# Performance work log

Hardware: AMD Instinct MI355X
Metric: run time of the kernel (lower is better)

Reference implementation:

```python
import jax, jax.numpy as jnp
import numpy as np

B, T, HID = 2, 1024, 1024
NQ, NK, DK, DV = 8, 4, 128, 128
KDIM, KKDIM, KVDIM, VDIM = NQ * DK, NK * DK, NK * DV, NQ * DV  # 1024, 512, 512, 1024
CONV_DIM = KDIM + KKDIM + KVDIM  # 2048
KSZ = 4
EPS = 1e-5


def setup_inputs() -> dict:
    ks = jax.random.split(jax.random.key(0), 6)
    tot = KDIM + KKDIM + KVDIM + VDIM + NQ + NQ  # 3104
    return {
        "x": jax.random.normal(ks[0], (B, T, HID), jnp.float32),
        "w_in": jax.random.normal(ks[1], (HID, tot), jnp.float32) * 0.02,
        "conv_w": jax.random.normal(ks[2], (CONV_DIM, KSZ), jnp.float32) * 0.3,
        "A_log": jax.random.uniform(ks[3], (NQ,), jnp.float32, 0.0, 1.0),
        "dt_bias": jnp.ones((NQ,), jnp.float32),
        "norm_w": jnp.ones((DV,), jnp.float32),
        "w_out": jax.random.normal(ks[4], (VDIM, HID), jnp.float32) * 0.02,
    }


def _l2norm(u):
    return u * jax.lax.rsqrt(jnp.sum(u * u, axis=-1, keepdims=True) + 1e-6)


def _forward(x, w_in, conv_w, A_log, dt_bias, norm_w, w_out):
    # merged input projection -> q | k | v | z(gate) | b(beta) | a(decay)
    mixed = x @ w_in  # [B,T,3104]
    o1, o2, o3, o4, o5 = KDIM, KDIM + KKDIM, KDIM + KKDIM + KVDIM, KDIM + KKDIM + KVDIM + VDIM, KDIM + KKDIM + KVDIM + VDIM + NQ
    q, k, v, z, b, a = jnp.split(mixed, [o1, o2, o3, o4, o5], axis=-1)

    # short causal depthwise conv over concatenated q,k,v + silu
    qkv = jnp.concatenate([q, k, v], axis=-1)  # [B,T,CONV_DIM]
    pad = jnp.pad(qkv, ((0, 0), (KSZ - 1, 0), (0, 0)))
    conv = sum(pad[:, j:j + T, :] * conv_w[:, j] for j in range(KSZ))
    qkv = jax.nn.silu(conv)
    q, k, v = jnp.split(qkv, [KDIM, KDIM + KKDIM], axis=-1)

    q = q.reshape(B, T, NQ, DK)
    k = k.reshape(B, T, NK, DK)
    v = v.reshape(B, T, NK, DV)
    # GQA: repeat kv heads to q heads (kv_proj_rank is None -> plain repeat)
    rep = NQ // NK
    k = jnp.repeat(k, rep, axis=2)
    v = jnp.repeat(v, rep, axis=2)

    # qk l2-norm in kernel + query scaling
    q = _l2norm(q) * (DK ** -0.5)
    k = _l2norm(k)

    beta = jax.nn.sigmoid(b)                                # [B,T,NQ]
    g = -jnp.exp(A_log) * jax.nn.softplus(a + dt_bias)      # [B,T,NQ] log-decay

    tm = lambda u: jnp.moveaxis(u, 1, 0)  # time-major for scan

    def step(S, inp):
        # S: [B,NQ,DK,DV]
        qt, kt, vt, gt, bt = inp
        S = S * jnp.exp(gt)[..., None, None]
        vt = bt[..., None] * (vt - jnp.einsum('bhk,bhkv->bhv', kt, S))
        S = S + kt[..., None] * vt[..., None, :]
        ot = jnp.einsum('bhk,bhkv->bhv', qt, S)
        return S, ot

    S0 = jnp.zeros((B, NQ, DK, DV), x.dtype)
    _, o = jax.lax.scan(step, S0, (tm(q), tm(k), tm(v), tm(g), tm(beta)))
    o = jnp.moveaxis(o, 0, 1)  # [B,T,NQ,DV]

    # gated RMS norm with z, then output projection
    zz = z.reshape(B, T, NQ, DV)
    o = o * jax.lax.rsqrt(jnp.mean(o * o, axis=-1, keepdims=True) + EPS)
    o = o * norm_w * jax.nn.silu(zz)
    return o.reshape(B, T, VDIM) @ w_out


def reference(x, w_in, conv_w, A_log, dt_bias, norm_w, w_out):
    return _forward(x, w_in, conv_w, A_log, dt_bias, norm_w, w_out)
```

## Files before the change

### kernel.cpp

```cpp
#include <hip/hip_runtime.h>
#include <hip/hip_bf16.h>
#include <math.h>

#define BB    2
#define TT    1024
#define HID   1024
#define NQ    8
#define NK    4
#define DK    128
#define DV    128
#define TOT   3088
#define CONVD 2048
#define KSZ   4
#define BT    (BB*TT)
#define CHUNK 64
#define NCHUNK (TT/CHUNK)
#define NBH   (BB*NQ)
#define NPAD1 3200
#define JW    32

typedef __attribute__((ext_vector_type(8))) short short8v;
typedef __attribute__((ext_vector_type(4))) float f32x4;
typedef unsigned short ushort_t;
typedef unsigned int uint_t;

__device__ __forceinline__ float siluf(float x)     { return x / (1.f + expf(-x)); }
__device__ __forceinline__ float sigmoidf_(float x) { return 1.f / (1.f + expf(-x)); }
__device__ __forceinline__ float softplusf_(float x){ return x > 15.f ? x : log1pf(expf(x)); }

__device__ __forceinline__ ushort_t f2bf(float f) {
    uint_t u = __builtin_bit_cast(uint_t, f);
    u = (u + 0x7fff + ((u >> 16) & 1)) >> 16;
    return (ushort_t)u;
}
__device__ __forceinline__ float bf2f(ushort_t u) {
    uint_t v = ((uint_t)u) << 16;
    return __builtin_bit_cast(float, v);
}
__device__ __forceinline__ ushort4 pack4(f32x4 v) {
    ushort4 p; p.x = f2bf(v[0]); p.y = f2bf(v[1]); p.z = f2bf(v[2]); p.w = f2bf(v[3]);
    return p;
}

__global__ __launch_bounds__(256) void f2bf_kernel(const float* __restrict__ src,
                                                   ushort_t* __restrict__ dst) {
    int i = (blockIdx.x * 256 + threadIdx.x) * 4;
    float4 v = *(const float4*)(src + i);
    ushort4 o;
    o.x = f2bf(v.x); o.y = f2bf(v.y); o.z = f2bf(v.z); o.w = f2bf(v.w);
    *(ushort4*)(dst + i) = o;
}

__global__ __launch_bounds__(256) void transpose_f2bf(const float* __restrict__ src,
                                                      ushort_t* __restrict__ dst,
                                                      int K, int N) {
    __shared__ float tile[32][33];
    int n0 = blockIdx.x * 32, k0 = blockIdx.y * 32;
    int c = threadIdx.x & 31, rbase = threadIdx.x >> 5;
    #pragma unroll
    for (int i = 0; i < 4; i++) {
        int r = rbase + i * 8;
        int n = n0 + c;
        tile[r][c] = (n < N) ? src[(size_t)(k0 + r) * N + n] : 0.f;
    }
    __syncthreads();
    #pragma unroll
    for (int i = 0; i < 4; i++) {
        int r = rbase + i * 8;
        dst[(size_t)(n0 + r) * K + k0 + c] = f2bf(tile[c][r]);
    }
}

__global__ __launch_bounds__(256) void gemm_bf16(const ushort_t* __restrict__ A,
                                                 const ushort_t* __restrict__ BTm,
                                                 float* __restrict__ C,
                                                 int K, int Nc, int ldc) {
    __shared__ ushort_t As[128 * 32];
    __shared__ ushort_t Bs[128 * 32];
    int tid = threadIdx.x;
    int wave = tid >> 6, lane = tid & 63;
    int wr = wave >> 1, wc = wave & 1;
    int row0 = blockIdx.y * 128, col0 = blockIdx.x * 128;

    f32x4 zero4 = {0.f, 0.f, 0.f, 0.f};
    f32x4 acc[4][4];
    #pragma unroll
    for (int m = 0; m < 4; m++)
        #pragma unroll
        for (int n = 0; n < 4; n++) acc[m][n] = zero4;

    int srow = wave * 32 + (lane >> 2);
    int koff = (lane & 3) * 8;
    const ushort_t* gA0 = A + (size_t)(row0 + srow) * K + koff;
    const ushort_t* gA1 = A + (size_t)(row0 + srow + 16) * K + koff;
    const ushort_t* gB0 = BTm + (size_t)(col0 + srow) * K + koff;
    const ushort_t* gB1 = BTm + (size_t)(col0 + srow + 16) * K + koff;
    ushort_t* lA0 = As + (wave * 2 + 0) * 512;
    ushort_t* lA1 = As + (wave * 2 + 1) * 512;
    ushort_t* lB0 = Bs + (wave * 2 + 0) * 512;
    ushort_t* lB1 = Bs + (wave * 2 + 1) * 512;

    for (int k0 = 0; k0 < K; k0 += 32) {
        __builtin_amdgcn_global_load_lds(
            (const __attribute__((address_space(1))) void*)(gA0 + k0),
            (__attribute__((address_space(3))) void*)lA0, 16, 0, 0);
        __builtin_amdgcn_global_load_lds(
            (const __attribute__((address_space(1))) void*)(gA1 + k0),
            (__attribute__((address_space(3))) void*)lA1, 16, 0, 0);
        __builtin_amdgcn_global_load_lds(
            (const __attribute__((address_space(1))) void*)(gB0 + k0),
            (__attribute__((address_space(3))) void*)lB0, 16, 0, 0);
        __builtin_amdgcn_global_load_lds(
            (const __attribute__((address_space(1))) void*)(gB1 + k0),
            (__attribute__((address_space(3))) void*)lB1, 16, 0, 0);
        __syncthreads();

        short8v af[4], bf[4];
        #pragma unroll
        for (int m = 0; m < 4; m++)
            af[m] = *(const short8v*)(As + (wr * 64 + m * 16 + (lane & 15)) * 32 + (lane >> 4) * 8);
        #pragma unroll
        for (int n = 0; n < 4; n++)
            bf[n] = *(const short8v*)(Bs + (wc * 64 + n * 16 + (lane & 15)) * 32 + (lane >> 4) * 8);
        #pragma unroll
        for (int m = 0; m < 4; m++)
            #pragma unroll
            for (int n = 0; n < 4; n++)
                acc[m][n] = __builtin_amdgcn_mfma_f32_16x16x32_bf16(af[m], bf[n], acc[m][n], 0, 0, 0);
        __syncthreads();
    }

    #pragma unroll
    for (int m = 0; m < 4; m++) {
        #pragma unroll
        for (int n = 0; n < 4; n++) {
            int row = row0 + wr * 64 + m * 16 + (lane >> 4) * 4;
            int col = col0 + wc * 64 + n * 16 + (lane & 15);
            if (col < Nc) {
                #pragma unroll
                for (int e = 0; e < 4; e++)
                    C[(size_t)(row + e) * ldc + col] = acc[m][n][e];
            }
        }
    }
}

__global__ __launch_bounds__(256) void conv_split_kernel(const float* __restrict__ mixed,
                                                         const float* __restrict__ conv_w,
                                                         const float* __restrict__ A_log,
                                                         const float* __restrict__ dt_bias,
                                                         ushort_t* __restrict__ qb,
                                                         ushort_t* __restrict__ kb,
                                                         float* __restrict__ kn,
                                                         float* __restrict__ vn,
                                                         float* __restrict__ beta,
                                                         float* __restrict__ g) {
    int bt = blockIdx.x;
    int t = bt & (TT - 1);
    int tid = threadIdx.x;
    int c0 = tid * 8;

    float val[8];
    #pragma unroll
    for (int i = 0; i < 8; i++) val[i] = 0.f;
    #pragma unroll
    for (int j = 0; j < KSZ; j++) {
        int tt = t - (KSZ - 1) + j;
        if (tt >= 0) {
            const float* src = mixed + (size_t)(bt - (KSZ - 1) + j) * TOT + c0;
            #pragma unroll
            for (int i = 0; i < 8; i++) val[i] += src[i] * conv_w[(c0 + i) * KSZ + j];
        }
    }
    #pragma unroll
    for (int i = 0; i < 8; i++) val[i] = siluf(val[i]);

    float ss = 0.f;
    #pragma unroll
    for (int i = 0; i < 8; i++) ss += val[i] * val[i];
    #pragma unroll
    for (int m = 1; m < 16; m <<= 1) ss += __shfl_xor(ss, m, 64);
    float rs = rsqrtf(ss + 1e-6f);

    if (tid < 128) {
        float sc = rs * 0.08838834764831845f;
        short8v pk;
        #pragma unroll
        for (int i = 0; i < 8; i++) pk[i] = (short)f2bf(val[i] * sc);
        *(short8v*)(qb + (size_t)bt * 1024 + c0) = pk;
    } else if (tid < 192) {
        int o = c0 - 1024;
        short8v pk;
        #pragma unroll
        for (int i = 0; i < 8; i++) {
            float kv = val[i] * rs;
            kn[(size_t)bt * 512 + o + i] = kv;
            pk[i] = (short)f2bf(kv);
        }
        *(short8v*)(kb + (size_t)bt * 512 + o) = pk;
    } else {
        #pragma unroll
        for (int i = 0; i < 8; i++) vn[(size_t)bt * 512 + (c0 - 1536) + i] = val[i];
    }
    if (tid < 8) {
        beta[bt * 8 + tid] = sigmoidf_(mixed[(size_t)bt * TOT + 3072 + tid]);
    } else if (tid < 16) {
        int h = tid - 8;
        g[bt * 8 + h] = -expf(A_log[h]) * softplusf_(mixed[(size_t)bt * TOT + 3080 + h] + dt_bias[h]);
    }
}

__global__ __launch_bounds__(256) void phaseA_kernel(const float* __restrict__ kn,
                                                     const float* __restrict__ vn,
                                                     const float* __restrict__ beta,
                                                     const float* __restrict__ g,
                                                     float* __restrict__ W,
                                                     ushort_t* __restrict__ Znegb,
                                                     ushort_t* __restrict__ knT,
                                                     float* __restrict__ Bvec) {
    int chunk = blockIdx.x;
    int bh = chunk >> 4, c = chunk & 15;
    int b = bh >> 3, h = bh & 7, hk = h >> 1;
    int bt0 = b * TT + c * CHUNK;
    int tid = threadIdx.x;
    int wave = tid >> 6, lane = tid & 63;
    int lr = lane & 15, lg = lane >> 4;

    __shared__ __align__(16) ushort_t kcb[64 * 128];
    __shared__ float Ms[64][65];
    __shared__ float Bv[64], Bev[64], bev[64];

    if (tid < 64) {
        float v = g[(size_t)(bt0 + tid) * 8 + h];
        #pragma unroll
        for (int off = 1; off < 64; off <<= 1) {
            float n = __shfl_up(v, off, 64);
            if (tid >= off) v += n;
        }
        Bv[tid] = v;
        Bev[tid] = expf(v);
        bev[tid] = beta[(size_t)(bt0 + tid) * 8 + h];
        Bvec[chunk * 64 + tid] = v;
    }
    for (int i = tid; i < 1024; i += 256) {
        int r = i >> 4, k16 = i & 15;
        const float* src = kn + (size_t)(bt0 + r) * 512 + hk * 128 + k16 * 8;
        float4 v0 = *(const float4*)src;
        float4 v1 = *(const float4*)(src + 4);
        short8v pk;
        pk[0] = (short)f2bf(v0.x); pk[1] = (short)f2bf(v0.y);
        pk[2] = (short)f2bf(v0.z); pk[3] = (short)f2bf(v0.w);
        pk[4] = (short)f2bf(v1.x); pk[5] = (short)f2bf(v1.y);
        pk[6] = (short)f2bf(v1.z); pk[7] = (short)f2bf(v1.w);
        int a = (r * 256 + k16 * 16) ^ ((r & 7) << 4);
        *(short8v*)((char*)kcb + a) = pk;
    }
    __syncthreads();

    {
        int t_lane = wave * 16 + lr;
        short8v af[4];
        #pragma unroll
        for (int ks = 0; ks < 4; ks++) {
            int a = (t_lane * 256 + ks * 64 + lg * 16) ^ ((t_lane & 7) << 4);
            af[ks] = *(const short8v*)((const char*)kcb + a);
        }
        for (int sb = 0; sb <= wave; sb++) {
            f32x4 macc = {0.f, 0.f, 0.f, 0.f};
            int s_lane = sb * 16 + lr;
            #pragma unroll
            for (int ks = 0; ks < 4; ks++) {
                int a = (s_lane * 256 + ks * 64 + lg * 16) ^ ((s_lane & 7) << 4);
                short8v bfr = *(const short8v*)((const char*)kcb + a);
                macc = __builtin_amdgcn_mfma_f32_16x16x32_bf16(af[ks], bfr, macc, 0, 0, 0);
            }
            #pragma unroll
            for (int e = 0; e < 4; e++) {
                int trow = wave * 16 + lg * 4 + e;
                int scol = sb * 16 + lr;
                Ms[trow][scol] = (scol < trow) ? macc[e] * bev[trow] * expf(Bv[trow] - Bv[scol]) : 0.f;
            }
        }
    }

    float Xr[64];
    if (tid < 128) {
        #pragma unroll
        for (int t = 0; t < 64; t++)
            Xr[t] = bev[t] * vn[(size_t)(bt0 + t) * 512 + hk * 128 + tid];
    } else {
        int r = tid - 128;
        #pragma unroll
        for (int t = 0; t < 64; t++)
            Xr[t] = bev[t] * Bev[t] * kn[(size_t)(bt0 + t) * 512 + hk * 128 + r];
    }
    __syncthreads();

    #pragma unroll
    for (int t = 1; t < 64; t++) {
        float a0 = 0.f, a1 = 0.f, a2 = 0.f, a3 = 0.f;
        #pragma unroll
        for (int s = 0; s + 4 <= t; s += 4) {
            a0 += Ms[t][s] * Xr[s];     a1 += Ms[t][s + 1] * Xr[s + 1];
            a2 += Ms[t][s + 2] * Xr[s + 2]; a3 += Ms[t][s + 3] * Xr[s + 3];
        }
        #pragma unroll
        for (int s = t & ~3; s < t; s++) a0 += Ms[t][s] * Xr[s];
        Xr[t] -= (a0 + a1) + (a2 + a3);
    }

    if (tid < 128) {
        float* Wc = W + (size_t)chunk * 8192 + tid;
        #pragma unroll
        for (int t = 0; t < 64; t++) Wc[t * 128] = Xr[t];
    } else {
        ushort_t* Zc = Znegb + (size_t)chunk * 8192 + (tid - 128);
        #pragma unroll
        for (int t = 0; t < 64; t++) Zc[t * 128] = f2bf(-Xr[t]);
    }

    if ((h & 1) == 0) {
        ushort_t* kT = knT + (size_t)(b * 4 + hk) * 131072 + c * 64;
        for (int i = tid; i < 8192; i += 256) {
            int r = i >> 6, tt = i & 63;
            int a = (tt * 256 + r * 2) ^ ((tt & 7) << 4);
            kT[(size_t)r * 1024 + tt] = *(const ushort_t*)((const char*)kcb + a);
        }
    }
}

__device__ __forceinline__ int swzSt(int j, int k) {
    int a = j * 256 + k * 2;
    return a ^ ((j & 7) << 4);
}
__device__ __forceinline__ int swzUt(int j, int s) {
    int a = j * 128 + s * 2;
    return a ^ ((j & 7) << 4);
}

__global__ __launch_bounds__(256) void phaseB_mfma(const ushort_t* __restrict__ knT,
                                                   const ushort_t* __restrict__ Znegb,
                                                   const float* __restrict__ W,
                                                   const float* __restrict__ Bvec,
                                                   ushort_t* __restrict__ SallT,
                                                   ushort_t* __restrict__ UTg) {
    int bh = blockIdx.x >> 2, cg = blockIdx.x & 3;
    int b = bh >> 3, h = bh & 7, hk = h >> 1;
    int j0 = cg * JW;
    int tid = threadIdx.x;
    int wave = tid >> 6, lane = tid & 63;
    int lr = lane & 15, lg = lane >> 4;

    __shared__ __align__(16) ushort_t St[JW * 128];
    __shared__ __align__(16) ushort_t Ut[JW * 64];
    __shared__ __align__(16) ushort_t ebs[2][64];
    __shared__ float b63s[2];

    for (int i = tid * 8; i < JW * 128; i += 2048)
        *(int4*)(St + i) = make_int4(0, 0, 0, 0);

    f32x4 Sacc[2][2];
    #pragma unroll
    for (int fr = 0; fr < 2; fr++)
        #pragma unroll
        for (int fc = 0; fc < 2; fc++) Sacc[fr][fc] = (f32x4){0.f, 0.f, 0.f, 0.f};

    const ushort_t* kTbase = knT + (size_t)(b * 4 + hk) * 131072;

    for (int c = 0; c < NCHUNK; c++) {
        int chunk = bh * 16 + c;
        int cb = c & 1;
        if (tid < 64) {
            float bv = Bvec[chunk * 64 + tid];
            float b63 = Bvec[chunk * 64 + 63];
            ebs[cb][tid] = f2bf(expf(b63 - bv));
            if (tid == 0) b63s[cb] = b63;
        }
        ushort_t* SgT = SallT + (size_t)chunk * 16384;
        #pragma unroll
        for (int fr = 0; fr < 2; fr++)
            #pragma unroll
            for (int fc = 0; fc < 2; fc++) {
                int r0 = wave * 32 + fr * 16 + lg * 4;
                int j = j0 + fc * 16 + lr;
                *(ushort4*)(SgT + (size_t)j * 128 + r0) = pack4(Sacc[fr][fc]);
            }
        __syncthreads();

        int t0 = wave * 16;
        const ushort_t* Zc = Znegb + (size_t)chunk * 8192;
        short8v za[4];
        #pragma unroll
        for (int ks = 0; ks < 4; ks++)
            za[ks] = *(const short8v*)(Zc + (size_t)(t0 + lr) * 128 + ks * 32 + lg * 8);
        const float* Wc = W + (size_t)chunk * 8192 + j0;
        f32x4 Uacc[2];
        #pragma unroll
        for (int fc = 0; fc < 2; fc++) {
            int j = fc * 16 + lr;
            #pragma unroll
            for (int e = 0; e < 4; e++)
                Uacc[fc][e] = Wc[(size_t)(t0 + lg * 4 + e) * 128 + j];
        }
        #pragma unroll
        for (int ks = 0; ks < 4; ks++)
            #pragma unroll
            for (int fc = 0; fc < 2; fc++) {
                short8v sb = *(const short8v*)((const char*)St + swzSt(fc * 16 + lr, ks * 32 + lg * 8));
                Uacc[fc] = __builtin_amdgcn_mfma_f32_16x16x32_bf16(za[ks], sb, Uacc[fc], 0, 0, 0);
            }
        ushort_t* UTc = UTg + (size_t)chunk * 8192;
        #pragma unroll
        for (int fc = 0; fc < 2; fc++) {
            int jl = fc * 16 + lr;
            ushort4 pu = pack4(Uacc[fc]);
            *(ushort4*)(UTc + (size_t)(j0 + jl) * 64 + t0 + lg * 4) = pu;
            *(ushort4*)((char*)Ut + swzUt(jl, t0 + lg * 4)) = pu;
        }
        float gC = expf(b63s[cb]);
        #pragma unroll
        for (int fr = 0; fr < 2; fr++)
            #pragma unroll
            for (int fc = 0; fc < 2; fc++)
                #pragma unroll
                for (int e = 0; e < 4; e++) Sacc[fr][fc][e] *= gC;
        __syncthreads();

        const ushort_t* kT = kTbase + c * 64;
        #pragma unroll
        for (int fr = 0; fr < 2; fr++) {
            int r = wave * 32 + fr * 16 + lr;
            #pragma unroll
            for (int ss = 0; ss < 2; ss++) {
                short8v ka = *(const short8v*)(kT + (size_t)r * 1024 + ss * 32 + lg * 8);
                short8v eb = *(const short8v*)(ebs[cb] + ss * 32 + lg * 8);
                short8v a;
                #pragma unroll
                for (int e = 0; e < 8; e++)
                    a[e] = (short)f2bf(bf2f((ushort_t)ka[e]) * bf2f((ushort_t)eb[e]));
                #pragma unroll
                for (int fc = 0; fc < 2; fc++) {
                    short8v ub = *(const short8v*)((const char*)Ut + swzUt(fc * 16 + lr, ss * 32 + lg * 8));
                    Sacc[fr][fc] = __builtin_amdgcn_mfma_f32_16x16x32_bf16(a, ub, Sacc[fr][fc], 0, 0, 0);
                }
            }
        }
        #pragma unroll
        for (int fr = 0; fr < 2; fr++)
            #pragma unroll
            for (int fc = 0; fc < 2; fc++) {
                int r = wave * 32 + fr * 16 + lg * 4;
                int j = fc * 16 + lr;
                *(ushort4*)((char*)St + swzSt(j, r)) = pack4(Sacc[fr][fc]);
            }
    }
}

__global__ __launch_bounds__(256) void phaseC_mfma(const ushort_t* __restrict__ qb,
                                                   const ushort_t* __restrict__ kb,
                                                   const ushort_t* __restrict__ UTg,
                                                   const ushort_t* __restrict__ SallT,
                                                   const float* __restrict__ Bvec,
                                                   float* __restrict__ o) {
    int chunk = blockIdx.x;
    int bh = chunk >> 4, c = chunk & 15;
    int b = bh >> 3, h = bh & 7, hk = h >> 1;
    int bt0 = b * TT + c * CHUNK;
    int tid = threadIdx.x, wave = tid >> 6, lane = tid & 63;
    int lr = lane & 15, lg = lane >> 4;

    __shared__ float Bv[64], Bev[64];
    __shared__ __align__(16) ushort_t Pb[64 * 64];

    if (tid < 64) { float v = Bvec[chunk * 64 + tid]; Bv[tid] = v; Bev[tid] = expf(v); }
    __syncthreads();

    int t_lane = wave * 16 + lr;
    const ushort_t* qrow = qb + (size_t)(bt0 + t_lane) * 1024 + h * 128;
    short8v qa[4];
    #pragma unroll
    for (int ks = 0; ks < 4; ks++) qa[ks] = *(const short8v*)(qrow + ks * 32 + lg * 8);

    #pragma unroll
    for (int sb = 0; sb < 4; sb++) {
        f32x4 pacc = {0.f, 0.f, 0.f, 0.f};
        const ushort_t* krow = kb + (size_t)(bt0 + sb * 16 + lr) * 512 + hk * 128;
        #pragma unroll
        for (int ks = 0; ks < 4; ks++) {
            short8v kf = *(const short8v*)(krow + ks * 32 + lg * 8);
            pacc = __builtin_amdgcn_mfma_f32_16x16x32_bf16(qa[ks], kf, pacc, 0, 0, 0);
        }
        int scol = sb * 16 + lr;
        #pragma unroll
        for (int e = 0; e < 4; e++) {
            int trow = wave * 16 + lg * 4 + e;
            float val = (scol <= trow) ? pacc[e] * expf(Bv[trow] - Bv[scol]) : 0.f;
            int a = (trow * 128 + scol * 2) ^ ((trow & 7) << 4);
            *(ushort_t*)((char*)Pb + a) = f2bf(val);
        }
    }

    float Ge[4];
    #pragma unroll
    for (int e = 0; e < 4; e++) Ge[e] = Bev[wave * 16 + lg * 4 + e];
    const ushort_t* ST = SallT + (size_t)chunk * 16384;
    f32x4 acc[8];
    #pragma unroll
    for (int n = 0; n < 8; n++) {
        acc[n] = (f32x4){0.f, 0.f, 0.f, 0.f};
        int j = n * 16 + lr;
        #pragma unroll
        for (int rs = 0; rs < 4; rs++) {
            short8v sf = *(const short8v*)(ST + (size_t)j * 128 + rs * 32 + lg * 8);
            acc[n] = __builtin_amdgcn_mfma_f32_16x16x32_bf16(qa[rs], sf, acc[n], 0, 0, 0);
        }
        #pragma unroll
        for (int e = 0; e < 4; e++) acc[n][e] *= Ge[e];
    }
    __syncthreads();

    short8v pa[2];
    #pragma unroll
    for (int ks = 0; ks < 2; ks++) {
        int a = (t_lane * 128 + (ks * 32 + lg * 8) * 2) ^ ((t_lane & 7) << 4);
        pa[ks] = *(const short8v*)((const char*)Pb + a);
    }
    const ushort_t* UTc = UTg + (size_t)chunk * 8192;
    #pragma unroll
    for (int n = 0; n < 8; n++) {
        int j = n * 16 + lr;
        #pragma unroll
        for (int ks = 0; ks < 2; ks++) {
            short8v uf = *(const short8v*)(UTc + (size_t)j * 64 + ks * 32 + lg * 8);
            acc[n] = __builtin_amdgcn_mfma_f32_16x16x32_bf16(pa[ks], uf, acc[n], 0, 0, 0);
        }
    }
    #pragma unroll
    for (int n = 0; n < 8; n++) {
        int j = n * 16 + lr;
        #pragma unroll
        for (int e = 0; e < 4; e++) {
            int t = wave * 16 + lg * 4 + e;
            o[(size_t)(bt0 + t) * 1024 + h * 128 + j] = acc[n][e];
        }
    }
}

__global__ __launch_bounds__(64) void norm_gate_kernel(const float* __restrict__ o_scan,
                                                       const float* __restrict__ mixed,
                                                       const float* __restrict__ norm_w,
                                                       ushort_t* __restrict__ ginb) {
    int bth = blockIdx.x;
    int bt = bth >> 3, h = bth & 7;
    int lane = threadIdx.x;
    size_t base = (size_t)bt * 1024 + h * 128;
    float o0 = o_scan[base + lane];
    float o1 = o_scan[base + lane + 64];
    float ss = o0 * o0 + o1 * o1;
    #pragma unroll
    for (int m = 1; m < 64; m <<= 1) ss += __shfl_xor(ss, m, 64);
    float r = rsqrtf(ss * (1.f / 128.f) + 1e-5f);
    size_t zbase = (size_t)bt * TOT + 2048 + h * 128;
    float z0 = mixed[zbase + lane];
    float z1 = mixed[zbase + lane + 64];
    ginb[base + lane]      = f2bf(o0 * r * norm_w[lane]      * siluf(z0));
    ginb[base + lane + 64] = f2bf(o1 * r * norm_w[lane + 64] * siluf(z1));
}

extern "C" void kernel_launch(void* const* d_in, const int* in_sizes, int n_in,
                              void* d_out, int out_size, void* d_ws, size_t ws_size,
                              hipStream_t stream) {
    const float* x       = (const float*)d_in[0];
    const float* w_in    = (const float*)d_in[1];
    const float* conv_w  = (const float*)d_in[2];
    const float* A_log   = (const float*)d_in[3];
    const float* dt_bias = (const float*)d_in[4];
    const float* norm_w  = (const float*)d_in[5];
    const float* w_out   = (const float*)d_in[6];
    float* out = (float*)d_out;

    float* ws = (float*)d_ws;
    float* mixed = ws;
    float* kn    = mixed + (size_t)BT * TOT;
    float* vn    = kn + (size_t)BT * 512;
    float* beta  = vn + (size_t)BT * 512;
    float* gdec  = beta + BT * 8;
    float* Wu    = gdec + BT * 8;
    float* Bvec  = Wu + (size_t)BT * 1024;
    float* qbf   = Bvec + NBH * NCHUNK * 64;
    float* kbf   = qbf + 1048576;
    float* knTf  = kbf + 524288;
    float* Znf   = knTf + 524288;
    float* UTf   = Znf + 1048576;
    float* SallTf= UTf + 1048576;
    float* bt2f  = SallTf + 2097152;

    ushort_t* qb    = (ushort_t*)qbf;
    ushort_t* kb    = (ushort_t*)kbf;
    ushort_t* knTb  = (ushort_t*)knTf;
    ushort_t* Znegb = (ushort_t*)Znf;
    ushort_t* UTb   = (ushort_t*)UTf;
    ushort_t* SallT = (ushort_t*)SallTf;
    ushort_t* bt2   = (ushort_t*)bt2f;
    ushort_t* xb    = (ushort_t*)SallTf;
    ushort_t* bt1   = (ushort_t*)knTf;
    ushort_t* ginb  = (ushort_t*)qbf;
    float* oscan    = Wu;

    f2bf_kernel<<<(BT * HID) / 1024, 256, 0, stream>>>(x, xb);
    transpose_f2bf<<<dim3(NPAD1 / 32, HID / 32), 256, 0, stream>>>(w_in, bt1, HID, TOT);
    transpose_f2bf<<<dim3(HID / 32, HID / 32), 256, 0, stream>>>(w_out, bt2, HID, HID);

    gemm_bf16<<<dim3(NPAD1 / 128, BT / 128), 256, 0, stream>>>(xb, bt1, mixed, HID, TOT, TOT);

    conv_split_kernel<<<BT, 256, 0, stream>>>(mixed, conv_w, A_log, dt_bias, qb, kb, kn, vn, beta, gdec);

    phaseA_kernel<<<NBH * NCHUNK, 256, 0, stream>>>(kn, vn, beta, gdec, Wu, Znegb, knTb, Bvec);
    phaseB_mfma<<<NBH * 4, 256, 0, stream>>>(knTb, Znegb, Wu, Bvec, SallT, UTb);
    phaseC_mfma<<<NBH * NCHUNK, 256, 0, stream>>>(qb, kb, UTb, SallT, Bvec, oscan);

    norm_gate_kernel<<<BT * NQ, 64, 0, stream>>>(oscan, mixed, norm_w, ginb);

    gemm_bf16<<<dim3(HID / 128, BT / 128), 256, 0, stream>>>(ginb, bt2, out, HID, HID, HID);
}
```

Baseline: 193.6 us.

## Prefetch next-chunk operands into registers in phaseB recurrence loop

Inside the sequential chunk loop of the phaseB state-recurrence kernel, the Z, W, k, and decay-vector loads for the next chunk are now issued early into registers, so global-memory latency overlaps the current chunk's MFMA work. The shared-memory decay-factor buffer is removed, and each lane now computes its own exp(b63 - b) values in registers instead of taking them from LDS as bf16. This raises register pressure and adds redundant exp calls per lane, but shortens the serial critical path of the recurrence.

```diff
diff --git a/kernel.cpp b/kernel.cpp
--- a/kernel.cpp
+++ b/kernel.cpp
@@ -350,11 +350,10 @@
     int tid = threadIdx.x;
     int wave = tid >> 6, lane = tid & 63;
     int lr = lane & 15, lg = lane >> 4;
+    int t0 = wave * 16;
 
     __shared__ __align__(16) ushort_t St[JW * 128];
     __shared__ __align__(16) ushort_t Ut[JW * 64];
-    __shared__ __align__(16) ushort_t ebs[2][64];
-    __shared__ float b63s[2];
 
     for (int i = tid * 8; i < JW * 128; i += 2048)
         *(int4*)(St + i) = make_int4(0, 0, 0, 0);
@@ -366,16 +365,37 @@
         for (int fc = 0; fc < 2; fc++) Sacc[fr][fc] = (f32x4){0.f, 0.f, 0.f, 0.f};
 
     const ushort_t* kTbase = knT + (size_t)(b * 4 + hk) * 131072;
+    int chunk0 = bh * 16;
+
+    short8v za[4], ka[4];
+    f32x4 wv[2];
+    f32x4 bvv[4];
+    float b63;
+    {
+        const ushort_t* Zc = Znegb + (size_t)chunk0 * 8192;
+        #pragma unroll
+        for (int ks = 0; ks < 4; ks++)
+            za[ks] = *(const short8v*)(Zc + (size_t)(t0 + lr) * 128 + ks * 32 + lg * 8);
+        const float* Wc = W + (size_t)chunk0 * 8192 + j0;
+        #pragma unroll
+        for (int fc = 0; fc < 2; fc++)
+            #pragma unroll
+            for (int e = 0; e < 4; e++)
+                wv[fc][e] = Wc[(size_t)(t0 + lg * 4 + e) * 128 + fc * 16 + lr];
+        #pragma unroll
+        for (int fr = 0; fr < 2; fr++)
+            #pragma unroll
+            for (int ss = 0; ss < 2; ss++)
+                ka[fr * 2 + ss] = *(const short8v*)(kTbase +
+                    (size_t)(wave * 32 + fr * 16 + lr) * 1024 + ss * 32 + lg * 8);
+        #pragma unroll
+        for (int q = 0; q < 4; q++)
+            bvv[q] = *(const f32x4*)(Bvec + chunk0 * 64 + (q >> 1) * 32 + lg * 8 + (q & 1) * 4);
+        b63 = Bvec[chunk0 * 64 + 63];
+    }
 
     for (int c = 0; c < NCHUNK; c++) {
-        int chunk = bh * 16 + c;
-        int cb = c & 1;
-        if (tid < 64) {
-            float bv = Bvec[chunk * 64 + tid];
-            float b63 = Bvec[chunk * 64 + 63];
-            ebs[cb][tid] = f2bf(expf(b63 - bv));
-            if (tid == 0) b63s[cb] = b63;
-        }
+        int chunk = chunk0 + c;
         ushort_t* SgT = SallT + (size_t)chunk * 16384;
         #pragma unroll
         for (int fr = 0; fr < 2; fr++)
@@ -385,23 +405,12 @@
                 int j = j0 + fc * 16 + lr;
                 *(ushort4*)(SgT + (size_t)j * 128 + r0) = pack4(Sacc[fr][fc]);
             }
+        f32x4 Uacc[2];
+        Uacc[0] = wv[0];
+        Uacc[1] = wv[1];
+
         __syncthreads();
 
-        int t0 = wave * 16;
-        const ushort_t* Zc = Znegb + (size_t)chunk * 8192;
-        short8v za[4];
-        #pragma unroll
-        for (int ks = 0; ks < 4; ks++)
-            za[ks] = *(const short8v*)(Zc + (size_t)(t0 + lr) * 128 + ks * 32 + lg * 8);
-        const float* Wc = W + (size_t)chunk * 8192 + j0;
-        f32x4 Uacc[2];
-        #pragma unroll
-        for (int fc = 0; fc < 2; fc++) {
-            int j = fc * 16 + lr;
-            #pragma unroll
-            for (int e = 0; e < 4; e++)
-                Uacc[fc][e] = Wc[(size_t)(t0 + lg * 4 + e) * 128 + j];
-        }
         #pragma unroll
         for (int ks = 0; ks < 4; ks++)
             #pragma unroll
@@ -417,33 +426,61 @@
             *(ushort4*)(UTc + (size_t)(j0 + jl) * 64 + t0 + lg * 4) = pu;
             *(ushort4*)((char*)Ut + swzUt(jl, t0 + lg * 4)) = pu;
         }
-        float gC = expf(b63s[cb]);
+        if (c + 1 < NCHUNK) {
+            const ushort_t* Zn = Znegb + (size_t)(chunk + 1) * 8192;
+            #pragma unroll
+            for (int ks = 0; ks < 4; ks++)
+                za[ks] = *(const short8v*)(Zn + (size_t)(t0 + lr) * 128 + ks * 32 + lg * 8);
+            const float* Wn = W + (size_t)(chunk + 1) * 8192 + j0;
+            #pragma unroll
+            for (int fc = 0; fc < 2; fc++)
+                #pragma unroll
+                for (int e = 0; e < 4; e++)
+                    wv[fc][e] = Wn[(size_t)(t0 + lg * 4 + e) * 128 + fc * 16 + lr];
+        }
+        float gC = expf(b63);
         #pragma unroll
         for (int fr = 0; fr < 2; fr++)
             #pragma unroll
             for (int fc = 0; fc < 2; fc++)
                 #pragma unroll
                 for (int e = 0; e < 4; e++) Sacc[fr][fc][e] *= gC;
+
         __syncthreads();
 
-        const ushort_t* kT = kTbase + c * 64;
+        float eb[2][8];
+        #pragma unroll
+        for (int ss = 0; ss < 2; ss++)
+            #pragma unroll
+            for (int e = 0; e < 8; e++)
+                eb[ss][e] = expf(b63 - bvv[ss * 2 + (e >> 2)][e & 3]);
+
         #pragma unroll
         for (int fr = 0; fr < 2; fr++) {
-            int r = wave * 32 + fr * 16 + lr;
             #pragma unroll
             for (int ss = 0; ss < 2; ss++) {
-                short8v ka = *(const short8v*)(kT + (size_t)r * 1024 + ss * 32 + lg * 8);
-                short8v eb = *(const short8v*)(ebs[cb] + ss * 32 + lg * 8);
                 short8v a;
                 #pragma unroll
                 for (int e = 0; e < 8; e++)
-                    a[e] = (short)f2bf(bf2f((ushort_t)ka[e]) * bf2f((ushort_t)eb[e]));
+                    a[e] = (short)f2bf(bf2f((ushort_t)ka[fr * 2 + ss][e]) * eb[ss][e]);
                 #pragma unroll
                 for (int fc = 0; fc < 2; fc++) {
                     short8v ub = *(const short8v*)((const char*)Ut + swzUt(fc * 16 + lr, ss * 32 + lg * 8));
                     Sacc[fr][fc] = __builtin_amdgcn_mfma_f32_16x16x32_bf16(a, ub, Sacc[fr][fc], 0, 0, 0);
                 }
             }
+        }
+        if (c + 1 < NCHUNK) {
+            #pragma unroll
+            for (int fr = 0; fr < 2; fr++)
+                #pragma unroll
+                for (int ss = 0; ss < 2; ss++)
+                    ka[fr * 2 + ss] = *(const short8v*)(kTbase +
+                        (size_t)(wave * 32 + fr * 16 + lr) * 1024 + (c + 1) * 64 + ss * 32 + lg * 8);
+            #pragma unroll
+            for (int q = 0; q < 4; q++)
+                bvv[q] = *(const f32x4*)(Bvec + (chunk + 1) * 64 + (q >> 1) * 32 + lg * 8 + (q & 1) * 4);
+            b63 = Bvec[(chunk + 1) * 64 + 63];
         }
         #pragma unroll
         for (int fr = 0; fr < 2; fr++)
```

Measured after the change: 186.2 us. 1.04x faster.

## Restructure chunk-state recurrence into single-wave blocks over 16-column slices

Applied to the files above, without the earlier changes.

The sequential inter-chunk state kernel now runs one wave per block, each owning a 16-column slice of the state, with twice as many blocks as before. Because each wave holds all 128 state rows, the __syncthreads barriers go away. Z, k and W loads for a chunk are issued up front to hide latency. The decay scaling moves from the k operand (per-element bf16 round trips) to the U tile in fp32 before it is written to shared memory. This trades more registers per lane and lower per-block parallelism for removing barriers and conversion work on the serial critical path.

```diff
diff --git a/kernel.cpp b/kernel.cpp
--- a/kernel.cpp
+++ b/kernel.cpp
@@ -17,7 +17,6 @@
 #define NCHUNK (TT/CHUNK)
 #define NBH   (BB*NQ)
 #define NPAD1 3200
-#define JW    32
 
 typedef __attribute__((ext_vector_type(8))) short short8v;
 typedef __attribute__((ext_vector_type(4))) float f32x4;
@@ -338,121 +337,103 @@
     return a ^ ((j & 7) << 4);
 }
 
-__global__ __launch_bounds__(256) void phaseB_mfma(const ushort_t* __restrict__ knT,
-                                                   const ushort_t* __restrict__ Znegb,
-                                                   const float* __restrict__ W,
-                                                   const float* __restrict__ Bvec,
-                                                   ushort_t* __restrict__ SallT,
-                                                   ushort_t* __restrict__ UTg) {
-    int bh = blockIdx.x >> 2, cg = blockIdx.x & 3;
+__global__ __launch_bounds__(64, 1) void phaseB_mfma(const ushort_t* __restrict__ knT,
+                                                     const ushort_t* __restrict__ Znegb,
+                                                     const float* __restrict__ W,
+                                                     const float* __restrict__ Bvec,
+                                                     ushort_t* __restrict__ SallT,
+                                                     ushort_t* __restrict__ UTg) {
+    int bh = blockIdx.x >> 3, cg = blockIdx.x & 7;
     int b = bh >> 3, h = bh & 7, hk = h >> 1;
-    int j0 = cg * JW;
-    int tid = threadIdx.x;
-    int wave = tid >> 6, lane = tid & 63;
+    int j0 = cg * 16;
+    int lane = threadIdx.x;
     int lr = lane & 15, lg = lane >> 4;
 
-    __shared__ __align__(16) ushort_t St[JW * 128];
-    __shared__ __align__(16) ushort_t Ut[JW * 64];
-    __shared__ __align__(16) ushort_t ebs[2][64];
-    __shared__ float b63s[2];
-
-    for (int i = tid * 8; i < JW * 128; i += 2048)
+    __shared__ __align__(16) ushort_t St[16 * 128];
+    __shared__ __align__(16) ushort_t Ut[16 * 64];
+
+    for (int i = lane * 8; i < 16 * 128; i += 512)
         *(int4*)(St + i) = make_int4(0, 0, 0, 0);
 
-    f32x4 Sacc[2][2];
-    #pragma unroll
-    for (int fr = 0; fr < 2; fr++)
-        #pragma unroll
-        for (int fc = 0; fc < 2; fc++) Sacc[fr][fc] = (f32x4){0.f, 0.f, 0.f, 0.f};
+    f32x4 Sacc[8];
+    #pragma unroll
+    for (int rb = 0; rb < 8; rb++) Sacc[rb] = (f32x4){0.f, 0.f, 0.f, 0.f};
 
     const ushort_t* kTbase = knT + (size_t)(b * 4 + hk) * 131072;
+    int chunk0 = bh * 16;
 
     for (int c = 0; c < NCHUNK; c++) {
-        int chunk = bh * 16 + c;
-        int cb = c & 1;
-        if (tid < 64) {
-            float bv = Bvec[chunk * 64 + tid];
-            float b63 = Bvec[chunk * 64 + 63];
-            ebs[cb][tid] = f2bf(expf(b63 - bv));
-            if (tid == 0) b63s[cb] = b63;
-        }
-        ushort_t* SgT = SallT + (size_t)chunk * 16384;
-        #pragma unroll
-        for (int fr = 0; fr < 2; fr++)
-            #pragma unroll
-            for (int fc = 0; fc < 2; fc++) {
-                int r0 = wave * 32 + fr * 16 + lg * 4;
-                int j = j0 + fc * 16 + lr;
-                *(ushort4*)(SgT + (size_t)j * 128 + r0) = pack4(Sacc[fr][fc]);
-            }
-        __syncthreads();
-
-        int t0 = wave * 16;
+        int chunk = chunk0 + c;
+        short8v za[4][4];
         const ushort_t* Zc = Znegb + (size_t)chunk * 8192;
-        short8v za[4];
-        #pragma unroll
-        for (int ks = 0; ks < 4; ks++)
-            za[ks] = *(const short8v*)(Zc + (size_t)(t0 + lr) * 128 + ks * 32 + lg * 8);
+        #pragma unroll
+        for (int tb = 0; tb < 4; tb++)
+            #pragma unroll
+            for (int ks = 0; ks < 4; ks++)
+                za[tb][ks] = *(const short8v*)(Zc + (size_t)(tb * 16 + lr) * 128 + ks * 32 + lg * 8);
+        short8v ka[8][2];
+        #pragma unroll
+        for (int rb = 0; rb < 8; rb++)
+            #pragma unroll
+            for (int ss = 0; ss < 2; ss++)
+                ka[rb][ss] = *(const short8v*)(kTbase +
+                    (size_t)(rb * 16 + lr) * 1024 + c * 64 + ss * 32 + lg * 8);
+        f32x4 wv[4];
         const float* Wc = W + (size_t)chunk * 8192 + j0;
-        f32x4 Uacc[2];
-        #pragma unroll
-        for (int fc = 0; fc < 2; fc++) {
-            int j = fc * 16 + lr;
+        #pragma unroll
+        for (int tb = 0; tb < 4; tb++)
             #pragma unroll
             for (int e = 0; e < 4; e++)
-                Uacc[fc][e] = Wc[(size_t)(t0 + lg * 4 + e) * 128 + j];
-        }
-        #pragma unroll
-        for (int ks = 0; ks < 4; ks++)
-            #pragma unroll
-            for (int fc = 0; fc < 2; fc++) {
-                short8v sb = *(const short8v*)((const char*)St + swzSt(fc * 16 + lr, ks * 32 + lg * 8));
-                Uacc[fc] = __builtin_amdgcn_mfma_f32_16x16x32_bf16(za[ks], sb, Uacc[fc], 0, 0, 0);
-            }
-        ushort_t* UTc = UTg + (size_t)chunk * 8192;
-        #pragma unroll
-        for (int fc = 0; fc < 2; fc++) {
-            int jl = fc * 16 + lr;
-            ushort4 pu = pack4(Uacc[fc]);
-            *(ushort4*)(UTc + (size_t)(j0 + jl) * 64 + t0 + lg * 4) = pu;
-            *(ushort4*)((char*)Ut + swzUt(jl, t0 + lg * 4)) = pu;
-        }
-        float gC = expf(b63s[cb]);
-        #pragma unroll
-        for (int fr = 0; fr < 2; fr++)
-            #pragma unroll
-            for (int fc = 0; fc < 2; fc++)
-                #pragma unroll
-                for (int e = 0; e < 4; e++) Sacc[fr][fc][e] *= gC;
-        __syncthreads();
-
-        const ushort_t* kT = kTbase + c * 64;
-        #pragma unroll
-        for (int fr = 0; fr < 2; fr++) {
-            int r = wave * 32 + fr * 16 + lr;
-            #pragma unroll
-            for (int ss = 0; ss < 2; ss++) {
-                short8v ka = *(const short8v*)(kT + (size_t)r * 1024 + ss * 32 + lg * 8);
-                short8v eb = *(const short8v*)(ebs[cb] + ss * 32 + lg * 8);
-                short8v a;
-                #pragma unroll
-                for (int e = 0; e < 8; e++)
-                    a[e] = (short)f2bf(bf2f((ushort_t)ka[e]) * bf2f((ushort_t)eb[e]));
-                #pragma unroll
-                for (int fc = 0; fc < 2; fc++) {
-                    short8v ub = *(const short8v*)((const char*)Ut + swzUt(fc * 16 + lr, ss * 32 + lg * 8));
-                    Sacc[fr][fc] = __builtin_amdgcn_mfma_f32_16x16x32_bf16(a, ub, Sacc[fr][fc], 0, 0, 0);
-                }
-            }
-        }
-        #pragma unroll
-        for (int fr = 0; fr < 2; fr++)
-            #pragma unroll
-            for (int fc = 0; fc < 2; fc++) {
-                int r = wave * 32 + fr * 16 + lg * 4;
-                int j = fc * 16 + lr;
-                *(ushort4*)((char*)St + swzSt(j, r)) = pack4(Sacc[fr][fc]);
-            }
+                wv[tb][e] = Wc[(size_t)(tb * 16 + lg * 4 + e) * 128 + lr];
+        f32x4 bvw[4];
+        #pragma unroll
+        for (int tb = 0; tb < 4; tb++)
+            bvw[tb] = *(const f32x4*)(Bvec + chunk * 64 + tb * 16 + lg * 4);
+        float b63 = Bvec[chunk * 64 + 63];
+
+        ushort_t* SgT = SallT + (size_t)chunk * 16384 + (size_t)(j0 + lr) * 128;
+        #pragma unroll
+        for (int rb = 0; rb < 8; rb++)
+            *(ushort4*)(SgT + rb * 16 + lg * 4) = pack4(Sacc[rb]);
+
+        f32x4 Uacc[4];
+        #pragma unroll
+        for (int tb = 0; tb < 4; tb++) Uacc[tb] = wv[tb];
+        #pragma unroll
+        for (int ks = 0; ks < 4; ks++) {
+            short8v sb = *(const short8v*)((const char*)St + swzSt(lr, ks * 32 + lg * 8));
+            #pragma unroll
+            for (int tb = 0; tb < 4; tb++)
+                Uacc[tb] = __builtin_amdgcn_mfma_f32_16x16x32_bf16(za[tb][ks], sb, Uacc[tb], 0, 0, 0);
+        }
+
+        ushort_t* UTc = UTg + (size_t)chunk * 8192 + (size_t)(j0 + lr) * 64;
+        #pragma unroll
+        for (int tb = 0; tb < 4; tb++) {
+            *(ushort4*)(UTc + tb * 16 + lg * 4) = pack4(Uacc[tb]);
+            f32x4 us;
+            #pragma unroll
+            for (int e = 0; e < 4; e++) us[e] = Uacc[tb][e] * expf(b63 - bvw[tb][e]);
+            *(ushort4*)((char*)Ut + swzUt(lr, tb * 16 + lg * 4)) = pack4(us);
+        }
+
+        float gC = expf(b63);
+        #pragma unroll
+        for (int rb = 0; rb < 8; rb++)
+            #pragma unroll
+            for (int e = 0; e < 4; e++) Sacc[rb][e] *= gC;
+
+        #pragma unroll
+        for (int ss = 0; ss < 2; ss++) {
+            short8v ub = *(const short8v*)((const char*)Ut + swzUt(lr, ss * 32 + lg * 8));
+            #pragma unroll
+            for (int rb = 0; rb < 8; rb++)
+                Sacc[rb] = __builtin_amdgcn_mfma_f32_16x16x32_bf16(ka[rb][ss], ub, Sacc[rb], 0, 0, 0);
+        }
+
+        #pragma unroll
+        for (int rb = 0; rb < 8; rb++)
+            *(ushort4*)((char*)St + swzSt(lr, rb * 16 + lg * 4)) = pack4(Sacc[rb]);
     }
 }
 
@@ -616,7 +597,7 @@
     conv_split_kernel<<<BT, 256, 0, stream>>>(mixed, conv_w, A_log, dt_bias, qb, kb, kn, vn, beta, gdec);
 
     phaseA_kernel<<<NBH * NCHUNK, 256, 0, stream>>>(kn, vn, beta, gdec, Wu, Znegb, knTb, Bvec);
-    phaseB_mfma<<<NBH * 4, 256, 0, stream>>>(knTb, Znegb, Wu, Bvec, SallT, UTb);
+    phaseB_mfma<<<NBH * 8, 64, 0, stream>>>(knTb, Znegb, Wu, Bvec, SallT, UTb);
     phaseC_mfma<<<NBH * NCHUNK, 256, 0, stream>>>(qb, kb, UTb, SallT, Bvec, oscan);
 
     norm_gate_kernel<<<BT * NQ, 64, 0, stream>>>(oscan, mixed, norm_w, ginb);
```

New measurement: 197.3 us. About the same (+1.9%).
